# Kernel tuning notes

Hardware: AMD Instinct MI355X
Metric: run time of the kernel (lower is better)

Reference implementation:

```python
import jax, jax.numpy as jnp
import numpy as np
import math
from jax import lax

S = 2048   # layer_size (number of neurons)
T = 384    # timesteps per forward call
ALPHA = 0.15
DT = 0.1
THRESH = -50.0
V_RESET = -70.0
VL = -70.0
GL = 0.025
CM = 0.5
TAU = CM / GL                                   # 20.0
COEF = DT ** ALPHA * math.gamma(2.0 - ALPHA) / CM  # dt^alpha * Gamma(2-alpha) / Cm


def setup_inputs() -> dict:
    key = jax.random.key(0)
    I_old = jax.random.normal(key, (S, T), dtype=jnp.float32)
    # class-level fractional (Grunwald-Letnikov style) weight vector, x=5000
    x = 5000
    nv = np.arange(x - 1)
    w = ((x - nv + 1) ** (1.0 - ALPHA) - (x - nv) ** (1.0 - ALPHA)).astype(np.float32)
    return {"I_old": I_old, "weights": jnp.asarray(w)}


def _forward(I_old, weights):
    S_, T_ = I_old.shape
    dtype = I_old.dtype
    # wr[a] = weights[-a]: the memory weight applied to a delta that is `a` steps old.
    # Original: np.inner(weights[-N+1:], delta_trace) pairs oldest delta with weights[-(N-1)]
    # and the newest delta with weights[-1].
    wr = jnp.concatenate([jnp.zeros((1,), dtype), weights[::-1][:T_].astype(dtype)])  # [T+1]
    jidx = jnp.arange(T_)  # buffer slot j holds the delta appended at global step j

    def step(carry, xs):
        V, buf = carry          # V: [S], buf: [S, T] delta history (slot j = delta of step j)
        n, I_n = xs             # n: scalar step index, I_n: [S]
        # fractional memory term: sum_{j=1}^{n-1} wr[n-j] * delta_j
        ages = n - jidx                                        # [T]
        coeff = jnp.where((ages >= 1) & (jidx >= 1),
                          wr[jnp.clip(ages, 0, T_)], jnp.zeros((), dtype))  # [T]
        memory = buf @ coeff                                   # [S]
        # three update rules depending on the global step counter
        V1 = V + (DT / TAU) * (-V + I_n / GL)                  # N == 1 branch
        V2 = COEF * (-GL * (V - VL) + I_n) + V - memory        # N >= 2 branch
        V_pre = jnp.where(n == 0, jnp.full_like(V, -70.0),
                          jnp.where(n == 1, V1, V2))
        spike = (V - THRESH > 0).astype(dtype)                 # spike uses PREVIOUS V
        reset = lax.stop_gradient(spike * (THRESH - V_RESET))  # detached reset
        V_new = V_pre - reset
        buf = buf.at[:, n].set(V_new - V)                      # append delta (n=0 slot masked out)
        return (V_new, buf), (spike, V_new)

    V0 = jnp.zeros((S_,), dtype)          # V_trace initialized to 0 per neuron
    buf0 = jnp.zeros((S_, T_), dtype)
    (_, _), (spk, trc) = lax.scan(step, (V0, buf0), (jnp.arange(T_), I_old.T))
    return spk.T, trc.T                    # each [S, T]


def reference(I_old, weights):
    return _forward(I_old, weights)
```

## Files before the change

kernel.cpp:

```cpp
#include <hip/hip_runtime.h>
#include <cmath>

#define T_STEPS 384
#define CH 64
#define NCH 6
#define WS 392

__device__ __forceinline__ float readlane_f(float v, int l) {
    return __int_as_float(__builtin_amdgcn_readlane(__float_as_int(v), l));
}

__device__ __forceinline__ float wave_shr1_f(float v) {
    return __int_as_float(__builtin_amdgcn_mov_dpp(__float_as_int(v), 0x138, 0xf, 0xf, true));
}

__global__ __launch_bounds__(128, 4)
void flif_kernel(const float* __restrict__ I_old, const float* __restrict__ W,
                 float* __restrict__ out, float cm1, float c2, float c3, int Stot)
{
    const int tid  = threadIdx.x;
    const int wid  = tid >> 6;
    const int lane = tid & 63;
    const int s    = blockIdx.x;

    __shared__ __align__(16) float wtr[4 * WS];
    __shared__ __align__(16) float dbuf[T_STEPS];
    __shared__ float accs[2][CH];

    for (int k = tid; k < 4 * WS; k += 128) {
        const int r = k / WS, kk = k - r * WS;
        const int i = kk + r;
        wtr[k] = (i <= 382) ? W[4998 - i] : 0.0f;
    }
    ((float*)accs)[tid] = 0.0f;
    __syncthreads();

    const int rl = lane & 3;
    const float* wlp = wtr + rl * WS + (lane - rl);

    if (wid == 1) {
        float A2 = 0.0f, A3 = 0.0f, A4 = 0.0f, A5 = 0.0f;
        #pragma unroll
        for (int c = 0; c < NCH; ++c) {
            if (c >= 1 && c <= 4) {
                const int src = c - 1;
                const float* dp = dbuf + src * CH;
                #pragma unroll
                for (int k = 0; k <= 60; k += 4) {
                    const float4 d4 = *reinterpret_cast<const float4*>(dp + k);
                    #pragma unroll
                    for (int t = c + 1; t <= 5; ++t) {
                        const int g = t - src;
                        const float4 w4 = *reinterpret_cast<const float4*>(wlp + (g * 64 - k - 4));
                        float& At = (t == 2) ? A2 : (t == 3) ? A3 : (t == 4) ? A4 : A5;
                        At = fmaf(d4.x, w4.w, At);
                        At = fmaf(d4.y, w4.z, At);
                        At = fmaf(d4.z, w4.y, At);
                        At = fmaf(d4.w, w4.x, At);
                    }
                }
                const float hand = (c == 1) ? A2 : (c == 2) ? A3 : (c == 3) ? A4 : A5;
                accs[(c + 1) & 1][lane] = hand;
            }
            __syncthreads();
        }
        return;
    }

    const float* Irow = I_old + (size_t)s * T_STEPS;
    float Inext = Irow[lane];
    const float w0   = (lane >= 1) ? W[4999 - lane] : 0.0f;
    const float wr1n = -W[4998];

    float V = 0.0f, d = 0.0f, b = 0.0f, P = 0.0f;
    float tcs[NCH], spks[NCH];

    for (int c = 0; c < NCH; ++c) {
        const int cb = c * CH;
        const float Ic = Inext;
        if (c + 1 < NCH) Inext = Irow[cb + CH + lane];

        float acc = (c == 0) ? 0.0f : accs[c & 1][lane];
        if (c >= 1) {
            const float* dp = dbuf + (c - 1) * CH;
            #pragma unroll
            for (int m0 = 60; m0 >= 0; m0 -= 4) {
                const float4 d4 = *reinterpret_cast<const float4*>(dp + (60 - m0));
                const float4 w4 = *reinterpret_cast<const float4*>(wlp + m0);
                acc = fmaf(d4.x, w4.w, acc);
                acc = fmaf(d4.y, w4.z, acc);
                acc = fmaf(d4.z, w4.y, acc);
                acc = fmaf(d4.w, w4.x, acc);
            }
        }

        float u = fmaf(c3, Ic, c2) - acc;
        const float Vs = V;
        float tc = 0.0f;
        float w = w0;

        auto body = [&](int i) {
            const float t = fmaf(wr1n, d, P);
            d = t + b;
            P = readlane_f(u, (i + 1) & 63);
            V = V + d;
            const float rv = (V > -50.0f) ? -20.0f : 0.0f;
            b = fmaf(cm1, V, rv);
            u = fmaf(-w, d, u);
            w = wave_shr1_f(w);
            tc = (lane == i) ? V : tc;
        };

        if (c == 0) {
            V = -90.0f;
            if (lane == 0) tc = V;
            w = wave_shr1_f(w);
            const float I1 = readlane_f(Ic, 1);
            const float V1 = fmaf(0.005f, (I1 / 0.025f) - V, V);
            const float d1 = V1 - V;
            P = readlane_f(u, 2);
            u = fmaf(-w, d1, u);
            w = wave_shr1_f(w);
            if (lane == 1) tc = V1;
            V = V1;
            d = d1;
            const float rv = (V > -50.0f) ? -20.0f : 0.0f;
            b = fmaf(cm1, V, rv);
            #pragma unroll
            for (int i = 2; i < CH; ++i) body(i);
        } else {
            d = 0.0f;
            P = readlane_f(u, 0);
            #pragma unroll
            for (int i = 0; i < CH; ++i) body(i);
        }

        float prev = __shfl_up(tc, 1);
        if (lane == 0) prev = Vs;
        spks[c] = (prev > -50.0f) ? 1.0f : 0.0f;
        float dd = tc - prev;
        if (c == 0 && lane == 0) dd = 0.0f;
        dbuf[cb + lane] = dd;
        tcs[c] = tc;
        __syncthreads();
    }

    float* out_spk = out + (size_t)s * T_STEPS;
    float* out_trc = out + (size_t)Stot * T_STEPS + (size_t)s * T_STEPS;
    #pragma unroll
    for (int c = 0; c < NCH; ++c) {
        out_spk[c * CH + lane] = spks[c];
        out_trc[c * CH + lane] = tcs[c];
    }
}

extern "C" void kernel_launch(void* const* d_in, const int* in_sizes, int n_in,
                              void* d_out, int out_size, void* d_ws, size_t ws_size,
                              hipStream_t stream) {
    const float* I = (const float*)d_in[0];
    const float* W = (const float*)d_in[1];
    float* out = (float*)d_out;
    const int S = in_sizes[0] / T_STEPS;

    const double COEF = std::pow(0.1, 0.15) * std::tgamma(1.85) / 0.5;
    const float c3  = (float)COEF;
    const float cm1 = (float)(-COEF * 0.025);
    const float c2  = (float)(COEF * 0.025 * -70.0);

    flif_kernel<<<S, 128, 0, stream>>>(I, W, out, cm1, c2, c3, S);
}
```

Baseline: 80.74 us.

## Add third helper wave to split off older-chunk memory sums from the critical path

Adds a third wavefront per block that computes the memory contribution from chunks at distance two or more. The existing helper wave now only adds the immediately preceding chunk's contribution to that partial sum before handing the result to the main wave. The aim is to shorten the helper work between barriers so the serial main wave waits less at each chunk boundary. In exchange the block grows from 128 to 192 threads and gains extra shared memory, which may reduce how many blocks fit per CU.

```diff
diff --git a/kernel.cpp b/kernel.cpp
--- a/kernel.cpp
+++ b/kernel.cpp
@@ -14,53 +14,72 @@
     return __int_as_float(__builtin_amdgcn_mov_dpp(__float_as_int(v), 0x138, 0xf, 0xf, true));
 }
 
-__global__ __launch_bounds__(128, 4)
+__global__ __launch_bounds__(192, 6)
 void flif_kernel(const float* __restrict__ I_old, const float* __restrict__ W,
                  float* __restrict__ out, float cm1, float c2, float c3, int Stot)
 {
     const int tid  = threadIdx.x;
-    const int wid  = tid >> 6;
+    const int wid  = tid / 64;
     const int lane = tid & 63;
     const int s    = blockIdx.x;
 
     __shared__ __align__(16) float wtr[4 * WS];
     __shared__ __align__(16) float dbuf[T_STEPS];
     __shared__ float accs[2][CH];
+    __shared__ float accsA[2][CH];
 
-    for (int k = tid; k < 4 * WS; k += 128) {
+    for (int k = tid; k < 4 * WS; k += 192) {
         const int r = k / WS, kk = k - r * WS;
         const int i = kk + r;
         wtr[k] = (i <= 382) ? W[4998 - i] : 0.0f;
     }
-    ((float*)accs)[tid] = 0.0f;
+    if (tid < 128) { ((float*)accs)[tid] = 0.0f; ((float*)accsA)[tid] = 0.0f; }
     __syncthreads();
 
     const int rl = lane & 3;
     const float* wlp = wtr + rl * WS + (lane - rl);
 
+    if (wid == 2) {
+        for (int c = 0; c < NCH; ++c) {
+            if (c >= 1 && c <= 3) {
+                const int t = c + 2;
+                float acc = 0.0f;
+                for (int src = 0; src <= c - 1; ++src) {
+                    const int g = t - src;
+                    const float* dp = dbuf + src * CH;
+                    #pragma unroll
+                    for (int k = 0; k <= 60; k += 4) {
+                        const float4 d4 = *reinterpret_cast<const float4*>(dp + k);
+                        const float4 w4 = *reinterpret_cast<const float4*>(wlp + (g * 64 - k - 4));
+                        acc = fmaf(d4.x, w4.w, acc);
+                        acc = fmaf(d4.y, w4.z, acc);
+                        acc = fmaf(d4.z, w4.y, acc);
+                        acc = fmaf(d4.w, w4.x, acc);
+                    }
+                }
+                accsA[t & 1][lane] = acc;
+            }
+            __syncthreads();
+        }
+        return;
+    }
+
     if (wid == 1) {
-        float A2 = 0.0f, A3 = 0.0f, A4 = 0.0f, A5 = 0.0f;
-        #pragma unroll
         for (int c = 0; c < NCH; ++c) {
             if (c >= 1 && c <= 4) {
-                const int src = c - 1;
-                const float* dp = dbuf + src * CH;
+                const int t = c + 1;
+                float acc = (t >= 3) ? accsA[t & 1][lane] : 0.0f;
+                const float* dp = dbuf + (t - 2) * CH;
                 #pragma unroll
                 for (int k = 0; k <= 60; k += 4) {
                     const float4 d4 = *reinterpret_cast<const float4*>(dp + k);
-                    #pragma unroll
-                    for (int t = c + 1; t <= 5; ++t) {
-                        const int g = t - src;
-                        const float4 w4 = *reinterpret_cast<const float4*>(wlp + (g * 64 - k - 4));
-                        float& At = (t == 2) ? A2 : (t == 3) ? A3 : (t == 4) ? A4 : A5;
-                        At = fmaf(d4.x, w4.w, At);
-                        At = fmaf(d4.y, w4.z, At);
-                        At = fmaf(d4.z, w4.y, At);
-                        At = fmaf(d4.w, w4.x, At);
-                    }
+                    const float4 w4 = *reinterpret_cast<const float4*>(wlp + (128 - k - 4));
+                    acc = fmaf(d4.x, w4.w, acc);
+                    acc = fmaf(d4.y, w4.z, acc);
+                    acc = fmaf(d4.z, w4.y, acc);
+                    acc = fmaf(d4.w, w4.x, acc);
                 }
-                const float hand = (c == 1) ? A2 : (c == 2) ? A3 : (c == 3) ? A4 : A5;
-                accs[(c + 1) & 1][lane] = hand;
+                accs[t & 1][lane] = acc;
             }
             __syncthreads();
         }
@@ -167,5 +186,5 @@
     const float cm1 = (float)(-COEF * 0.025);
     const float c2  = (float)(COEF * 0.025 * -70.0);
 
-    flif_kernel<<<S, 128, 0, stream>>>(I, W, out, cm1, c2, c3, S);
+    flif_kernel<<<S, 192, 0, stream>>>(I, W, out, cm1, c2, c3, S);
 }
```

Measured after the change: 93.95 us. +16.4%, slower.

## Process two neurons per block with interleaved independent recurrences for ILP

Applied to the files above, without the earlier changes.

Each block now handles two neurons, running both serial scan chains in the same wave and interleaving their instructions so the latency of the dependent readlane/fma chain of one neuron hides the other's. Shared weights are loaded once per block, and the helper wave computes lookahead memory sums for both neurons. The grid is halved and launch bounds are relaxed, which raises register pressure and lowers the number of resident blocks. It also assumes S is even.

```diff
diff --git a/kernel.cpp b/kernel.cpp
--- a/kernel.cpp
+++ b/kernel.cpp
@@ -14,18 +14,19 @@
     return __int_as_float(__builtin_amdgcn_mov_dpp(__float_as_int(v), 0x138, 0xf, 0xf, true));
 }
 
-__global__ __launch_bounds__(128, 4)
+__global__ __launch_bounds__(128, 2)
 void flif_kernel(const float* __restrict__ I_old, const float* __restrict__ W,
                  float* __restrict__ out, float cm1, float c2, float c3, int Stot)
 {
     const int tid  = threadIdx.x;
     const int wid  = tid >> 6;
     const int lane = tid & 63;
-    const int s    = blockIdx.x;
+    const int nA   = 2 * blockIdx.x;
+    const int nB   = nA + 1;
 
     __shared__ __align__(16) float wtr[4 * WS];
-    __shared__ __align__(16) float dbuf[T_STEPS];
-    __shared__ float accs[2][CH];
+    __shared__ __align__(16) float dbuf[2][T_STEPS];
+    __shared__ float accs[2][2][CH];
 
     for (int k = tid; k < 4 * WS; k += 128) {
         const int r = k / WS, kk = k - r * WS;
@@ -33,124 +34,149 @@
         wtr[k] = (i <= 382) ? W[4998 - i] : 0.0f;
     }
     ((float*)accs)[tid] = 0.0f;
+    ((float*)accs)[tid + 128] = 0.0f;
     __syncthreads();
 
     const int rl = lane & 3;
     const float* wlp = wtr + rl * WS + (lane - rl);
 
     if (wid == 1) {
-        float A2 = 0.0f, A3 = 0.0f, A4 = 0.0f, A5 = 0.0f;
+        float A2a = 0, A3a = 0, A4a = 0, A5a = 0;
+        float A2b = 0, A3b = 0, A4b = 0, A5b = 0;
         #pragma unroll
         for (int c = 0; c < NCH; ++c) {
             if (c >= 1 && c <= 4) {
                 const int src = c - 1;
-                const float* dp = dbuf + src * CH;
                 #pragma unroll
-                for (int k = 0; k <= 60; k += 4) {
-                    const float4 d4 = *reinterpret_cast<const float4*>(dp + k);
+                for (int X = 0; X < 2; ++X) {
+                    const float* dp = dbuf[X] + src * CH;
                     #pragma unroll
-                    for (int t = c + 1; t <= 5; ++t) {
-                        const int g = t - src;
-                        const float4 w4 = *reinterpret_cast<const float4*>(wlp + (g * 64 - k - 4));
-                        float& At = (t == 2) ? A2 : (t == 3) ? A3 : (t == 4) ? A4 : A5;
-                        At = fmaf(d4.x, w4.w, At);
-                        At = fmaf(d4.y, w4.z, At);
-                        At = fmaf(d4.z, w4.y, At);
-                        At = fmaf(d4.w, w4.x, At);
+                    for (int k = 0; k <= 60; k += 4) {
+                        const float4 d4 = *reinterpret_cast<const float4*>(dp + k);
+                        #pragma unroll
+                        for (int t = c + 1; t <= 5; ++t) {
+                            const int g = t - src;
+                            const float4 w4 = *reinterpret_cast<const float4*>(wlp + (g * 64 - k - 4));
+                            float& At = (X == 0)
+                                ? ((t == 2) ? A2a : (t == 3) ? A3a : (t == 4) ? A4a : A5a)
+                                : ((t == 2) ? A2b : (t == 3) ? A3b : (t == 4) ? A4b : A5b);
+                            At = fmaf(d4.x, w4.w, At);
+                            At = fmaf(d4.y, w4.z, At);
+                            At = fmaf(d4.z, w4.y, At);
+                            At = fmaf(d4.w, w4.x, At);
+                        }
                     }
+                    const float hand = (X == 0)
+                        ? ((c == 1) ? A2a : (c == 2) ? A3a : (c == 3) ? A4a : A5a)
+                        : ((c == 1) ? A2b : (c == 2) ? A3b : (c == 3) ? A4b : A5b);
+                    accs[X][(c + 1) & 1][lane] = hand;
                 }
-                const float hand = (c == 1) ? A2 : (c == 2) ? A3 : (c == 3) ? A4 : A5;
-                accs[(c + 1) & 1][lane] = hand;
             }
             __syncthreads();
         }
         return;
     }
 
-    const float* Irow = I_old + (size_t)s * T_STEPS;
-    float Inext = Irow[lane];
+    const float* IrowA = I_old + (size_t)nA * T_STEPS;
+    const float* IrowB = I_old + (size_t)nB * T_STEPS;
+    float InextA = IrowA[lane];
+    float InextB = IrowB[lane];
     const float w0   = (lane >= 1) ? W[4999 - lane] : 0.0f;
     const float wr1n = -W[4998];
 
-    float V = 0.0f, d = 0.0f, b = 0.0f, P = 0.0f;
-    float tcs[NCH], spks[NCH];
+    float VA = 0, dA = 0, bA = 0, PA = 0;
+    float VB = 0, dB = 0, bB = 0, PB = 0;
+    float tcsA[NCH], spksA[NCH], tcsB[NCH], spksB[NCH];
 
     for (int c = 0; c < NCH; ++c) {
         const int cb = c * CH;
-        const float Ic = Inext;
-        if (c + 1 < NCH) Inext = Irow[cb + CH + lane];
+        const float IcA = InextA, IcB = InextB;
+        if (c + 1 < NCH) { InextA = IrowA[cb + CH + lane]; InextB = IrowB[cb + CH + lane]; }
 
-        float acc = (c == 0) ? 0.0f : accs[c & 1][lane];
+        float accA = (c == 0) ? 0.0f : accs[0][c & 1][lane];
+        float accB = (c == 0) ? 0.0f : accs[1][c & 1][lane];
         if (c >= 1) {
-            const float* dp = dbuf + (c - 1) * CH;
+            const float* dpA = dbuf[0] + (c - 1) * CH;
+            const float* dpB = dbuf[1] + (c - 1) * CH;
             #pragma unroll
             for (int m0 = 60; m0 >= 0; m0 -= 4) {
-                const float4 d4 = *reinterpret_cast<const float4*>(dp + (60 - m0));
                 const float4 w4 = *reinterpret_cast<const float4*>(wlp + m0);
-                acc = fmaf(d4.x, w4.w, acc);
-                acc = fmaf(d4.y, w4.z, acc);
-                acc = fmaf(d4.z, w4.y, acc);
-                acc = fmaf(d4.w, w4.x, acc);
+                const float4 a4 = *reinterpret_cast<const float4*>(dpA + (60 - m0));
+                const float4 b4 = *reinterpret_cast<const float4*>(dpB + (60 - m0));
+                accA = fmaf(a4.x, w4.w, accA);  accB = fmaf(b4.x, w4.w, accB);
+                accA = fmaf(a4.y, w4.z, accA);  accB = fmaf(b4.y, w4.z, accB);
+                accA = fmaf(a4.z, w4.y, accA);  accB = fmaf(b4.z, w4.y, accB);
+                accA = fmaf(a4.w, w4.x, accA);  accB = fmaf(b4.w, w4.x, accB);
             }
         }
 
-        float u = fmaf(c3, Ic, c2) - acc;
-        const float Vs = V;
-        float tc = 0.0f;
-        float w = w0;
+        float uA = fmaf(c3, IcA, c2) - accA;
+        float uB = fmaf(c3, IcB, c2) - accB;
+        const float VsA = VA, VsB = VB;
+        float tcA = 0.0f, tcB = 0.0f;
+        float wA = w0, wB = w0;
 
         auto body = [&](int i) {
-            const float t = fmaf(wr1n, d, P);
-            d = t + b;
-            P = readlane_f(u, (i + 1) & 63);
-            V = V + d;
-            const float rv = (V > -50.0f) ? -20.0f : 0.0f;
-            b = fmaf(cm1, V, rv);
-            u = fmaf(-w, d, u);
-            w = wave_shr1_f(w);
-            tc = (lane == i) ? V : tc;
+            const float tA = fmaf(wr1n, dA, PA);         const float tB = fmaf(wr1n, dB, PB);
+            dA = tA + bA;                                dB = tB + bB;
+            PA = readlane_f(uA, (i + 1) & 63);           PB = readlane_f(uB, (i + 1) & 63);
+            VA = VA + dA;                                VB = VB + dB;
+            const float rA = (VA > -50.0f) ? -20.0f : 0.0f;
+            const float rB = (VB > -50.0f) ? -20.0f : 0.0f;
+            bA = fmaf(cm1, VA, rA);                      bB = fmaf(cm1, VB, rB);
+            uA = fmaf(-wA, dA, uA);                      uB = fmaf(-wB, dB, uB);
+            wA = wave_shr1_f(wA);                        wB = wave_shr1_f(wB);
+            tcA = (lane == i) ? VA : tcA;                tcB = (lane == i) ? VB : tcB;
         };
 
         if (c == 0) {
-            V = -90.0f;
-            if (lane == 0) tc = V;
-            w = wave_shr1_f(w);
-            const float I1 = readlane_f(Ic, 1);
-            const float V1 = fmaf(0.005f, (I1 / 0.025f) - V, V);
-            const float d1 = V1 - V;
-            P = readlane_f(u, 2);
-            u = fmaf(-w, d1, u);
-            w = wave_shr1_f(w);
-            if (lane == 1) tc = V1;
-            V = V1;
-            d = d1;
-            const float rv = (V > -50.0f) ? -20.0f : 0.0f;
-            b = fmaf(cm1, V, rv);
+            VA = -90.0f; VB = -90.0f;
+            if (lane == 0) { tcA = VA; tcB = VB; }
+            wA = wave_shr1_f(wA); wB = wave_shr1_f(wB);
+            const float I1A = readlane_f(IcA, 1);
+            const float I1B = readlane_f(IcB, 1);
+            const float V1A = fmaf(0.005f, (I1A / 0.025f) - VA, VA);
+            const float V1B = fmaf(0.005f, (I1B / 0.025f) - VB, VB);
+            const float d1A = V1A - VA, d1B = V1B - VB;
+            PA = readlane_f(uA, 2); PB = readlane_f(uB, 2);
+            uA = fmaf(-wA, d1A, uA); uB = fmaf(-wB, d1B, uB);
+            wA = wave_shr1_f(wA); wB = wave_shr1_f(wB);
+            if (lane == 1) { tcA = V1A; tcB = V1B; }
+            VA = V1A; VB = V1B; dA = d1A; dB = d1B;
+            bA = fmaf(cm1, VA, (VA > -50.0f) ? -20.0f : 0.0f);
+            bB = fmaf(cm1, VB, (VB > -50.0f) ? -20.0f : 0.0f);
             #pragma unroll
             for (int i = 2; i < CH; ++i) body(i);
         } else {
-            d = 0.0f;
-            P = readlane_f(u, 0);
+            dA = 0.0f; dB = 0.0f;
+            PA = readlane_f(uA, 0); PB = readlane_f(uB, 0);
             #pragma unroll
             for (int i = 0; i < CH; ++i) body(i);
         }
 
-        float prev = __shfl_up(tc, 1);
-        if (lane == 0) prev = Vs;
-        spks[c] = (prev > -50.0f) ? 1.0f : 0.0f;
-        float dd = tc - prev;
-        if (c == 0 && lane == 0) dd = 0.0f;
-        dbuf[cb + lane] = dd;
-        tcs[c] = tc;
+        float prevA = __shfl_up(tcA, 1);
+        float prevB = __shfl_up(tcB, 1);
+        if (lane == 0) { prevA = VsA; prevB = VsB; }
+        spksA[c] = (prevA > -50.0f) ? 1.0f : 0.0f;
+        spksB[c] = (prevB > -50.0f) ? 1.0f : 0.0f;
+        float ddA = tcA - prevA, ddB = tcB - prevB;
+        if (c == 0 && lane == 0) { ddA = 0.0f; ddB = 0.0f; }
+        dbuf[0][cb + lane] = ddA;
+        dbuf[1][cb + lane] = ddB;
+        tcsA[c] = tcA; tcsB[c] = tcB;
         __syncthreads();
     }
 
-    float* out_spk = out + (size_t)s * T_STEPS;
-    float* out_trc = out + (size_t)Stot * T_STEPS + (size_t)s * T_STEPS;
+    float* spkA = out + (size_t)nA * T_STEPS;
+    float* spkB = out + (size_t)nB * T_STEPS;
+    float* trcA = out + (size_t)Stot * T_STEPS + (size_t)nA * T_STEPS;
+    float* trcB = out + (size_t)Stot * T_STEPS + (size_t)nB * T_STEPS;
     #pragma unroll
     for (int c = 0; c < NCH; ++c) {
-        out_spk[c * CH + lane] = spks[c];
-        out_trc[c * CH + lane] = tcs[c];
+        spkA[c * CH + lane] = spksA[c];
+        spkB[c * CH + lane] = spksB[c];
+        trcA[c * CH + lane] = tcsA[c];
+        trcB[c * CH + lane] = tcsB[c];
     }
 }
 
@@ -167,5 +193,5 @@
     const float cm1 = (float)(-COEF * 0.025);
     const float c2  = (float)(COEF * 0.025 * -70.0);
 
-    flif_kernel<<<S, 128, 0, stream>>>(I, W, out, cm1, c2, c3, S);
+    flif_kernel<<<S / 2, 128, 0, stream>>>(I, W, out, cm1, c2, c3, S);
 }
```

Result: slower. 140.8 us (+74.4%).

## Speculate no-spike chunks with a two-step recurrence and fall back on threshold

Applied to the files above, without the earlier changes.

Each 64-step chunk now runs a speculative path that assumes no spike resets. This lets the serial recurrence be rewritten in terms of the two previous deltas, with the cm1*V feedback folded into the coefficients. That removes the per-step compare/select from the critical dependency chain and splits the readlane prefetch across two alternating registers. If any lane's trace comes within a margin of the threshold, the chunk is recomputed with the original exact loop. This adds a wave-wide vote and more code size, and in the worst case runs both paths.

```diff
diff --git a/kernel.cpp b/kernel.cpp
--- a/kernel.cpp
+++ b/kernel.cpp
@@ -9,7 +9,6 @@
 __device__ __forceinline__ float readlane_f(float v, int l) {
     return __int_as_float(__builtin_amdgcn_readlane(__float_as_int(v), l));
 }
-
 __device__ __forceinline__ float wave_shr1_f(float v) {
     return __int_as_float(__builtin_amdgcn_mov_dpp(__float_as_int(v), 0x138, 0xf, 0xf, true));
 }
@@ -69,10 +68,14 @@
 
     const float* Irow = I_old + (size_t)s * T_STEPS;
     float Inext = Irow[lane];
-    const float w0   = (lane >= 1) ? W[4999 - lane] : 0.0f;
+    const float w0seed = (lane >= 1) ? W[4999 - lane] : 0.0f;
     const float wr1n = -W[4998];
-
-    float V = 0.0f, d = 0.0f, b = 0.0f, P = 0.0f;
+    const float b1 = cm1 - W[4998];
+    const float b2 = cm1 - W[4997];
+    const float w2seed = (lane >= 1) ? (cm1 - W[4999 - lane]) : 0.0f;
+
+    float Vcs = 0.0f;
+    float rvprev = 0.0f;
     float tcs[NCH], spks[NCH];
 
     for (int c = 0; c < NCH; ++c) {
@@ -94,46 +97,114 @@
             }
         }
 
-        float u = fmaf(c3, Ic, c2) - acc;
-        const float Vs = V;
+        const float u0 = fmaf(c3, Ic, c2) - acc;
+        const float Vs = Vcs;
         float tc = 0.0f;
-        float w = w0;
-
-        auto body = [&](int i) {
-            const float t = fmaf(wr1n, d, P);
-            d = t + b;
-            P = readlane_f(u, (i + 1) & 63);
-            V = V + d;
-            const float rv = (V > -50.0f) ? -20.0f : 0.0f;
-            b = fmaf(cm1, V, rv);
-            u = fmaf(-w, d, u);
-            w = wave_shr1_f(w);
-            tc = (lane == i) ? V : tc;
-        };
-
-        if (c == 0) {
-            V = -90.0f;
-            if (lane == 0) tc = V;
-            w = wave_shr1_f(w);
-            const float I1 = readlane_f(Ic, 1);
-            const float V1 = fmaf(0.005f, (I1 / 0.025f) - V, V);
-            const float d1 = V1 - V;
-            P = readlane_f(u, 2);
-            u = fmaf(-w, d1, u);
-            w = wave_shr1_f(w);
-            if (lane == 1) tc = V1;
-            V = V1;
-            d = d1;
-            const float rv = (V > -50.0f) ? -20.0f : 0.0f;
-            b = fmaf(cm1, V, rv);
-            #pragma unroll
-            for (int i = 2; i < CH; ++i) body(i);
-        } else {
-            d = 0.0f;
-            P = readlane_f(u, 0);
-            #pragma unroll
-            for (int i = 0; i < CH; ++i) body(i);
-        }
+        float Vend;
+
+        {
+            float u, S, Pq0, Pq1, w2;
+            float dm1 = 0.0f, dm2 = 0.0f;
+            if (c == 0) {
+                float V0 = -90.0f;
+                if (lane == 0) tc = V0;
+                const float wf = wave_shr1_f(w0seed);
+                const float I1 = readlane_f(Ic, 1);
+                const float V1 = fmaf(0.005f, (I1 / 0.025f) - V0, V0);
+                const float d1 = V1 - V0;
+                const float ue = fmaf(-wf, d1, u0);
+                if (lane == 1) tc = V1;
+                u = fmaf(cm1, V1, ue);
+                S = V1;
+                Pq0 = readlane_f(u, 2);
+                Pq1 = readlane_f(u, 3);
+                w2 = wave_shr1_f(wave_shr1_f(w2seed));
+                #pragma unroll
+                for (int i = 2; i < CH; ++i) {
+                    const float x  = fmaf(b2, dm2, (i & 1) ? Pq1 : Pq0);
+                    const float dn = fmaf(b1, dm1, x);
+                    const float nf = readlane_f(u, (i + 2) & 63);
+                    if (i & 1) Pq1 = nf; else Pq0 = nf;
+                    u = fmaf(w2, dn, u);
+                    w2 = wave_shr1_f(w2);
+                    S += dn;
+                    tc = (lane == i) ? S : tc;
+                    dm2 = dm1; dm1 = dn;
+                }
+                Vend = S;
+            } else {
+                u = fmaf(cm1, Vcs, u0);
+                S = 0.0f;
+                Pq0 = readlane_f(u, 0) + rvprev;
+                Pq1 = readlane_f(u, 1);
+                w2 = w2seed;
+                #pragma unroll
+                for (int i = 0; i < CH; ++i) {
+                    const float x  = fmaf(b2, dm2, (i & 1) ? Pq1 : Pq0);
+                    const float dn = fmaf(b1, dm1, x);
+                    const float nf = readlane_f(u, (i + 2) & 63);
+                    if (i & 1) Pq1 = nf; else Pq0 = nf;
+                    u = fmaf(w2, dn, u);
+                    w2 = wave_shr1_f(w2);
+                    S += dn;
+                    tc = (lane == i) ? S : tc;
+                    dm2 = dm1; dm1 = dn;
+                }
+                tc = Vcs + tc;
+                Vend = Vcs + S;
+            }
+        }
+
+        if (__any(tc > -50.5f)) {
+            float V, d, b, P, w;
+            float tcf = 0.0f;
+            float uf = u0;
+            if (c == 0) {
+                V = -90.0f;
+                if (lane == 0) tcf = V;
+                w = wave_shr1_f(w0seed);
+                const float I1 = readlane_f(Ic, 1);
+                const float V1 = fmaf(0.005f, (I1 / 0.025f) - V, V);
+                const float d1 = V1 - V;
+                P = readlane_f(uf, 2);
+                uf = fmaf(-w, d1, uf);
+                w = wave_shr1_f(w);
+                if (lane == 1) tcf = V1;
+                V = V1; d = d1;
+                b = fmaf(cm1, V, (V > -50.0f) ? -20.0f : 0.0f);
+                #pragma unroll
+                for (int i = 2; i < CH; ++i) {
+                    const float t = fmaf(wr1n, d, P);
+                    d = t + b;
+                    P = readlane_f(uf, (i + 1) & 63);
+                    V = V + d;
+                    const float rv = (V > -50.0f) ? -20.0f : 0.0f;
+                    b = fmaf(cm1, V, rv);
+                    uf = fmaf(-w, d, uf);
+                    w = wave_shr1_f(w);
+                    tcf = (lane == i) ? V : tcf;
+                }
+            } else {
+                V = Vcs; d = 0.0f;
+                b = fmaf(cm1, Vcs, rvprev);
+                w = w0seed;
+                P = readlane_f(uf, 0);
+                #pragma unroll
+                for (int i = 0; i < CH; ++i) {
+                    const float t = fmaf(wr1n, d, P);
+                    d = t + b;
+                    P = readlane_f(uf, (i + 1) & 63);
+                    V = V + d;
+                    const float rv = (V > -50.0f) ? -20.0f : 0.0f;
+                    b = fmaf(cm1, V, rv);
+                    uf = fmaf(-w, d, uf);
+                    w = wave_shr1_f(w);
+                    tcf = (lane == i) ? V : tcf;
+                }
+            }
+            tc = tcf; Vend = V;
+        }
+        rvprev = (Vend > -50.0f) ? -20.0f : 0.0f;
 
         float prev = __shfl_up(tc, 1);
         if (lane == 0) prev = Vs;
@@ -142,6 +213,7 @@
         if (c == 0 && lane == 0) dd = 0.0f;
         dbuf[cb + lane] = dd;
         tcs[c] = tc;
+        Vcs = Vend;
         __syncthreads();
     }
 
```

Measured after the change: 76.23 us. 1.06x faster.
